# Kernel tuning notes

Hardware: AMD Instinct MI355X
Metric: run time of the kernel (lower is better)

## Reference

```python
import jax, jax.numpy as jnp
import numpy as np

IMG_H, IMG_W = 128, 128
FOCAL, NEAR, FAR = 140.0, 0.1, 10.0
RIGHT = (IMG_W - 1.0) / 2.0 * NEAR / FOCAL
TOP = RIGHT * (float(IMG_H) / IMG_W)
# row-vector GL perspective projection (v_clip = v_cam @ P), matching dirt's matrices.perspective_projection
PROJ = np.array([
    [NEAR / RIGHT, 0.0, 0.0, 0.0],
    [0.0, NEAR / TOP, 0.0, 0.0],
    [0.0, 0.0, -(FAR + NEAR) / (FAR - NEAR), -1.0],
    [0.0, 0.0, -2.0 * FAR * NEAR / (FAR - NEAR), 0.0],
], dtype=np.float32)
CHUNK = 64
EPS = 1e-9


def transform_vertices(vertices, pose):
    # vertices [N,3], pose [4,4] -> clip-space coords [N,4]
    G = jnp.array([[1.0, 0.0, 0.0], [0.0, -1.0, 0.0], [0.0, 0.0, -1.0]], jnp.float32)
    rot = G @ pose[:3, :3]
    cam_pose = pose.at[:3, :3].set(rot)
    cam_pose = cam_pose.at[1, 3].set(-pose[1, 3]).at[2, 3].set(-pose[2, 3])
    view = cam_pose.T
    vh = jnp.concatenate([vertices, jnp.ones_like(vertices[:, :1])], axis=1)
    return (vh @ view) @ jnp.asarray(PROJ)


def screen_coords(clip):
    # clip [...,4] -> pixel x (right), pixel y (down), ndc z, clip w
    w = clip[..., 3]
    x = (clip[..., 0] / w * 0.5 + 0.5) * IMG_W
    y = (0.5 - clip[..., 1] / w * 0.5) * IMG_H
    z = clip[..., 2] / w
    return x, y, z, w


def select_faces(clip, faces):
    # hard z-buffer visibility pass: per pixel, id of nearest covering face (-1 = background)
    B = clip.shape[0]
    F = faces.shape[0]
    px = jnp.arange(IMG_W, dtype=jnp.float32) + 0.5            # [W]
    py = (jnp.arange(IMG_H, dtype=jnp.float32) + 0.5)[:, None]  # [H,1]
    x, y, z, w = screen_coords(clip)                            # each [B,N]
    fchunks = faces.reshape(F // CHUNK, CHUNK, 3)
    idchunks = jnp.arange(F, dtype=jnp.int32).reshape(F // CHUNK, CHUNK)

    def body(carry, xs):
        best_z, best_f = carry
        fc, fid = xs                                  # [C,3], [C]
        xi, yi, zi, wi = x[:, fc], y[:, fc], z[:, fc], w[:, fc]   # [B,C,3]
        e4 = lambda a: a[..., None, None]             # [B,C] -> [B,C,1,1]
        x0, x1, x2 = e4(xi[..., 0]), e4(xi[..., 1]), e4(xi[..., 2])
        y0, y1, y2 = e4(yi[..., 0]), e4(yi[..., 1]), e4(yi[..., 2])
        # edge functions at pixel centers -> unnormalized barycentrics [B,C,H,W]
        e0 = (x2 - x1) * (py - y1) - (y2 - y1) * (px - x1)
        e1 = (x0 - x2) * (py - y2) - (y0 - y2) * (px - x2)
        e2 = (x1 - x0) * (py - y0) - (y1 - y0) * (px - x0)
        area = e0 + e1 + e2
        s = jnp.sign(area)
        ok = (jnp.abs(area) > EPS) & e4((wi > 1e-6).all(-1))
        inside = (e0 * s >= 0) & (e1 * s >= 0) & (e2 * s >= 0) & ok
        zpix = (e0 * e4(zi[..., 0]) + e1 * e4(zi[..., 1]) + e2 * e4(zi[..., 2])) / jnp.where(jnp.abs(area) > EPS, area, 1.0)
        inside = inside & (zpix >= -1.0) & (zpix <= 1.0)
        zc = jnp.where(inside, zpix, jnp.inf)         # [B,C,H,W]
        zmin = zc.min(axis=1)                         # [B,H,W]
        fsel = fid[zc.argmin(axis=1)]                 # [B,H,W]
        better = zmin < best_z
        return (jnp.where(better, zmin, best_z), jnp.where(better, fsel, best_f)), None

    init = (jnp.full((B, IMG_H, IMG_W), jnp.inf, jnp.float32),
            jnp.full((B, IMG_H, IMG_W), -1, jnp.int32))
    (_, best_f), _ = jax.lax.scan(body, init, (fchunks, idchunks))
    return best_f


def shade(clip, vcolors, faces, face_id):
    # differentiable perspective-correct interpolation of [mask,u,v] for the visible face
    fid = jnp.maximum(face_id, 0)                       # [B,H,W]
    vidx = faces[fid]                                   # [B,H,W,3]
    tri = jax.vmap(lambda c, vi: c[vi])(clip, vidx)     # [B,H,W,3,4]
    col = jax.vmap(lambda c, vi: c[vi])(vcolors, vidx)  # [B,H,W,3,3]
    x, y, z, w = screen_coords(tri)                     # [B,H,W,3]
    px = (jnp.arange(IMG_W, dtype=jnp.float32) + 0.5)[None, None, :]
    py = (jnp.arange(IMG_H, dtype=jnp.float32) + 0.5)[None, :, None]
    e0 = (x[..., 2] - x[..., 1]) * (py - y[..., 1]) - (y[..., 2] - y[..., 1]) * (px - x[..., 1])
    e1 = (x[..., 0] - x[..., 2]) * (py - y[..., 2]) - (y[..., 0] - y[..., 2]) * (px - x[..., 2])
    e2 = (x[..., 1] - x[..., 0]) * (py - y[..., 0]) - (y[..., 1] - y[..., 0]) * (px - x[..., 0])
    b = jnp.stack([e0, e1, e2], axis=-1)                # [B,H,W,3]
    bw = b / w                                          # perspective-correct weights
    denom = bw.sum(-1, keepdims=True)
    denom = jnp.where(jnp.abs(denom) > EPS, denom, 1.0)
    pc = bw / denom
    gbuffer = (pc[..., None] * col).sum(axis=-2)        # [B,H,W,3]
    mask = (face_id >= 0).astype(jnp.float32)[..., None]
    return gbuffer * mask


def sample_texture(texture, uv):
    # texture [TH,TW,C], uv [H,W,2]; faithful to original: clip uv, scale by full texture shape, bilinear
    th, tw = texture.shape[0], texture.shape[1]
    idx = jnp.clip(uv[..., ::-1], 0.0, 1.0) * jnp.array([th, tw], jnp.float32)
    fl = jnp.floor(idx)
    frac = idx - fl
    i = fl.astype(jnp.int32)
    iy0 = jnp.clip(i[..., 0], 0, th - 1)
    iy1 = jnp.clip(i[..., 0] + 1, 0, th - 1)
    ix0 = jnp.clip(i[..., 1], 0, tw - 1)
    ix1 = jnp.clip(i[..., 1] + 1, 0, tw - 1)
    tl = texture[iy0, ix0]; tr = texture[iy0, ix1]
    bl = texture[iy1, ix0]; br = texture[iy1, ix1]
    fy = frac[..., :1]; fx = frac[..., 1:]
    return (tl * (1.0 - fx) * (1.0 - fy) + tr * fx * (1.0 - fy)
            + bl * (1.0 - fx) * fy + br * fx * fy)


def forward(vertices, uv_map, faces, texture, poses):
    faces = faces.astype(jnp.int32)
    clip = jax.vmap(transform_vertices)(vertices, poses)         # [B,N,4]
    vcolors = jnp.concatenate([jnp.ones_like(vertices[..., :1]), uv_map], axis=-1)  # [B,N,3] = [1,u,v]
    face_id = select_faces(jax.lax.stop_gradient(clip), faces)   # [B,H,W]
    gbuffer = shade(clip, vcolors, faces, face_id)               # [B,H,W,3]
    mask_render = gbuffer[..., :1]
    uv = gbuffer[..., 1:3]
    unlit = jax.vmap(sample_texture)(texture, uv)                # [B,H,W,3]
    return unlit * mask_render


def setup_inputs():
    key = jax.random.key(0)
    k = jax.random.split(key, 5)
    B, N, F, TH, TW = 4, 4096, 8192, 2048, 2048
    vertices = jax.random.uniform(k[0], (B, N, 3), jnp.float32, -0.5, 0.5)
    uv_map = jax.random.uniform(k[1], (B, N, 2), jnp.float32)
    faces = jax.random.randint(k[2], (F, 3), 0, N, jnp.int32)
    texture = jax.random.uniform(k[3], (B, TH, TW, 3), jnp.float32)
    poses = jnp.tile(jnp.eye(4, dtype=jnp.float32)[None], (B, 1, 1))
    poses = poses.at[:, 2, 3].set(3.0)  # object ends up ~3 units in front of the GL camera
    poses = poses.at[:, 0, 3].set(jax.random.uniform(k[4], (B,), jnp.float32, -0.2, 0.2))
    return {"vertices": vertices, "uv_map": uv_map, "faces": faces, "texture": texture, "poses": poses}


def reference(vertices, uv_map, faces, texture, poses):
    return forward(vertices, uv_map, faces, texture, poses)
```

## Files before the change

### kernel.cpp

```cpp
#include <hip/hip_runtime.h>
#include <cstdint>
#include <cmath>

#define IMG_H 128
#define IMG_W 128
#define TILE 16
#define TILES_X (IMG_W / TILE)
#define TILES_Y (IMG_H / TILE)
#define NTILES (TILES_X * TILES_Y)
#define NSUB 8
#define CCH 128

constexpr double FOCAL_D = 140.0, NEAR_D = 0.1, FAR_D = 10.0;
constexpr double RIGHT_D = (IMG_W - 1.0) / 2.0 * NEAR_D / FOCAL_D;
constexpr double TOP_D   = RIGHT_D * ((double)IMG_H / (double)IMG_W);
constexpr float P00 = (float)(NEAR_D / RIGHT_D);
constexpr float P11 = (float)(NEAR_D / TOP_D);
constexpr float P22 = (float)(-(FAR_D + NEAR_D) / (FAR_D - NEAR_D));
constexpr float P32 = (float)(-2.0 * FAR_D * NEAR_D / (FAR_D - NEAR_D));

__device__ __forceinline__ unsigned long long packKey(float z, int f) {
    unsigned int zb = __float_as_uint(z);
    zb = (zb & 0x80000000u) ? ~zb : (zb | 0x80000000u);
    return ((unsigned long long)zb << 32) | (unsigned int)f;
}

__device__ __forceinline__ bool edgeAllOut(float dx, float dy, float ax, float ay,
                                           float px0, float px1, float py0, float py1,
                                           float s) {
#pragma clang fp contract(off)
    bool all = true;
    #pragma unroll
    for (int c = 0; c < 4; ++c) {
        float px = (c & 1) ? px1 : px0;
        float py = (c & 2) ? py1 : py0;
        float e = dx * (py - ay) - dy * (px - ax);
        float T = fabsf(dx) * (fabsf(py) + fabsf(ay)) + fabsf(dy) * (fabsf(px) + fabsf(ax));
        float m = 1e-5f * T + 1e-3f;
        all = all && (e * s < -m);
    }
    return all;
}

__global__ void k_vertex(const float* __restrict__ verts, const float* __restrict__ poses,
                         float4* __restrict__ vscr, int* __restrict__ cnt, int cntN,
                         int B, int N) {
#pragma clang fp contract(off)
    int id = blockIdx.x * blockDim.x + threadIdx.x;
    if (cnt && id < cntN) cnt[id] = 0;
    if (id >= B * N) return;
    int b = id / N;
    const float* v = verts + (size_t)id * 3;
    const float* P = poses + (size_t)b * 16;
    float x = v[0], y = v[1], z = v[2];
    float cp[4][4] = {
        { P[0],  P[1],  P[2],  P[3]  },
        {-P[4], -P[5], -P[6], -P[7]  },
        {-P[8], -P[9], -P[10],-P[11] },
        { P[12], P[13], P[14], P[15] }
    };
    float cam[4];
    for (int j = 0; j < 4; ++j)
        cam[j] = ((x * cp[j][0] + y * cp[j][1]) + z * cp[j][2]) + cp[j][3];
    float c0 = cam[0] * P00;
    float c1 = cam[1] * P11;
    float c2 = (cam[2] * P22) + (cam[3] * P32);
    float c3 = cam[2] * (-1.0f);
    float sx = ((c0 / c3) * 0.5f + 0.5f) * (float)IMG_W;
    float sy = (0.5f - (c1 / c3) * 0.5f) * (float)IMG_H;
    float sz = c2 / c3;
    vscr[id] = make_float4(sx, sy, sz, c3);
}

__global__ void k_bin(const int* __restrict__ faces, const float4* __restrict__ vscr,
                      float4* __restrict__ recA, float4* __restrict__ recB,
                      float4* __restrict__ recC, float4* __restrict__ recD,
                      int* __restrict__ list, int* __restrict__ cnt,
                      unsigned long long* __restrict__ keybuf,
                      int B, int N, int F) {
#pragma clang fp contract(off)
    int id = blockIdx.x * blockDim.x + threadIdx.x;
    for (int i = id; i < B * IMG_H * IMG_W; i += B * F) keybuf[i] = ~0ull;
    if (id >= B * F) return;
    int b = id / F, f = id - b * F;
    int i0 = faces[f * 3 + 0], i1 = faces[f * 3 + 1], i2 = faces[f * 3 + 2];
    float4 v0 = vscr[(size_t)b * N + i0];
    float4 v1 = vscr[(size_t)b * N + i1];
    float4 v2 = vscr[(size_t)b * N + i2];

    if (!(v0.w > 1e-6f && v1.w > 1e-6f && v2.w > 1e-6f)) return;

    float minx = fminf(v0.x, fminf(v1.x, v2.x));
    float maxx = fmaxf(v0.x, fmaxf(v1.x, v2.x));
    float miny = fminf(v0.y, fminf(v1.y, v2.y));
    float maxy = fmaxf(v0.y, fmaxf(v1.y, v2.y));
    if (!(minx <= maxx) || !(miny <= maxy)) return;
    minx = fmaxf(minx, -4.0f);  maxx = fminf(maxx, (float)IMG_W + 4.0f);
    miny = fmaxf(miny, -4.0f);  maxy = fminf(maxy, (float)IMG_H + 4.0f);
    int xlo = max(0, (int)floorf(minx) - 1);
    int xhi = min(IMG_W - 1, (int)floorf(maxx) + 1);
    int ylo = max(0, (int)floorf(miny) - 1);
    int yhi = min(IMG_H - 1, (int)floorf(maxy) + 1);
    if (xlo > xhi || ylo > yhi) return;

    float dx0 = v2.x - v1.x, dy0 = v2.y - v1.y;
    float dx1 = v0.x - v2.x, dy1 = v0.y - v2.y;
    float dx2 = v1.x - v0.x, dy2 = v1.y - v0.y;

    size_t r = (size_t)id;
    unsigned pb = (unsigned)xlo | ((unsigned)xhi << 8) | ((unsigned)ylo << 16) | ((unsigned)yhi << 24);
    recA[r] = make_float4(v1.x, v1.y, v2.x, v2.y);
    recB[r] = make_float4(v0.x, v0.y, 0.0f, 0.0f);
    recC[r] = make_float4(v0.z, v1.z, v2.z, __uint_as_float(pb));
    recD[r] = make_float4(dx0, dy0, dx1, dy1);

    int tx0 = xlo >> 4, tx1 = xhi >> 4, ty0 = ylo >> 4, ty1 = yhi >> 4;
    int sub = f & (NSUB - 1);
    int cap = (F + NSUB - 1) / NSUB;
    for (int ty = ty0; ty <= ty1; ++ty) {
        float py0 = (float)(ty << 4) + 0.5f, py1 = py0 + 15.0f;
        for (int tx = tx0; tx <= tx1; ++tx) {
            float px0 = (float)(tx << 4) + 0.5f, px1 = px0 + 15.0f;
            float ea = dx0 * (py0 - v1.y) - dy0 * (px0 - v1.x);
            float eb = dx1 * (py0 - v2.y) - dy1 * (px0 - v2.x);
            float ec = dx2 * (py0 - v0.y) - dy2 * (px0 - v0.x);
            float areaC = (ea + eb) + ec;
            float Tm = (fabsf(dx0) + fabsf(dx1) + fabsf(dx2)) * 300.0f
                     + (fabsf(dy0) + fabsf(dy1) + fabsf(dy2)) * 300.0f;
            float mA = 1e-5f * Tm + 1e-2f;
            bool cull = false;
            if (fabsf(areaC) > mA) {
                float s = (areaC > 0.0f) ? 1.0f : -1.0f;
                cull = edgeAllOut(dx0, dy0, v1.x, v1.y, px0, px1, py0, py1, s)
                    || edgeAllOut(dx1, dy1, v2.x, v2.y, px0, px1, py0, py1, s)
                    || edgeAllOut(dx2, dy2, v0.x, v0.y, px0, px1, py0, py1, s);
            }
            if (cull) continue;
            int bin = b * NTILES + ty * TILES_X + tx;
            int slot = atomicAdd(&cnt[bin * NSUB + sub], 1);
            list[((size_t)bin * NSUB + sub) * cap + slot] = f;
        }
    }
}

__global__ __launch_bounds__(256) void k_rasterChunk(const int* __restrict__ list,
        const int* __restrict__ cnt,
        const float4* __restrict__ recA, const float4* __restrict__ recB,
        const float4* __restrict__ recC, const float4* __restrict__ recD,
        unsigned long long* __restrict__ keybuf, int B, int F, int cap) {
#pragma clang fp contract(off)
    int ls = blockIdx.x;
    int n = cnt[ls];
    int base = blockIdx.y * CCH;
    if (base >= n) return;
    int m = min(CCH, n - base);
    int bin = ls >> 3;
    int b = bin / NTILES;
    int tile = bin - b * NTILES;
    const int* mylist = list + (size_t)ls * cap + base;

    int tx = tile & (TILES_X - 1), ty = tile >> 3;
    int t = threadIdx.x;
    int wv = t >> 6;
    int wx0 = (tx << 4) + ((wv & 1) << 3);
    int wy0 = (ty << 4) + ((wv >> 1) << 3);
    int x = wx0 + (t & 7);
    int y = wy0 + ((t >> 3) & 7);
    float px = (float)x + 0.5f, py = (float)y + 0.5f;
    int wx1 = wx0 + 7, wy1 = wy0 + 7;

    unsigned long long key = ~0ull;

    __shared__ float4 sA[CCH], sB[CCH], sC[CCH], sD[CCH];
    __shared__ int sfid[CCH];

    if (t < m) {
        int f = mylist[t];
        sfid[t] = f;
        size_t r = (size_t)b * F + f;
        sA[t] = recA[r]; sB[t] = recB[r]; sC[t] = recC[r]; sD[t] = recD[r];
    }
    __syncthreads();

    for (int j = 0; j < m; ++j) {
        float4 cc = sC[j];
        unsigned pb = __float_as_uint(cc.w);
        int fxlo = (int)(pb & 0xFFu), fxhi = (int)((pb >> 8) & 0xFFu);
        int fylo = (int)((pb >> 16) & 0xFFu), fyhi = (int)(pb >> 24);
        if (fxhi < wx0 || fxlo > wx1 || fyhi < wy0 || fylo > wy1) continue;
        float4 aa = sA[j], bb = sB[j], dd = sD[j];
        float e0 = dd.x * (py - aa.y) - dd.y * (px - aa.x);
        float e1 = dd.z * (py - aa.w) - dd.w * (px - aa.z);
        float dx2 = aa.x - bb.x, dy2 = aa.y - bb.y;
        float e2 = dx2 * (py - bb.y) - dy2 * (px - bb.x);
        float area = (e0 + e1) + e2;
        bool okA = fabsf(area) > 1e-9f;
        float s = (area > 0.0f) ? 1.0f : ((area < 0.0f) ? -1.0f : area);
        bool inside = (e0 * s >= 0.0f) && (e1 * s >= 0.0f) && (e2 * s >= 0.0f) && okA;
        if (__ballot(inside)) {
            float den = okA ? area : 1.0f;
            float zpix = ((e0 * cc.x + e1 * cc.y) + e2 * cc.z) / den;
            if (inside && (zpix >= -1.0f) && (zpix <= 1.0f)) {
                unsigned long long k = packKey(zpix, sfid[j]);
                key = (k < key) ? k : key;
            }
        }
    }
    if (key != ~0ull) {
        unsigned long long* ap = &keybuf[(size_t)b * (IMG_H * IMG_W) + (size_t)y * IMG_W + x];
        atomicMin(ap, key);
    }
}

__global__ __launch_bounds__(256) void k_rasterF(const int* __restrict__ faces,
                                                 const float4* __restrict__ vscr,
                                                 unsigned long long* __restrict__ keybuf,
                                                 int B, int N, int F) {
#pragma clang fp contract(off)
    int wid = __builtin_amdgcn_readfirstlane(blockIdx.x * 4 + (threadIdx.x >> 6));
    if (wid >= B * F) return;
    int b = wid / F;
    int f = wid - b * F;
    int lane = threadIdx.x & 63;

    int i0 = faces[f * 3 + 0], i1 = faces[f * 3 + 1], i2 = faces[f * 3 + 2];
    float4 v0 = vscr[(size_t)b * N + i0];
    float4 v1 = vscr[(size_t)b * N + i1];
    float4 v2 = vscr[(size_t)b * N + i2];
    if (!(v0.w > 1e-6f && v1.w > 1e-6f && v2.w > 1e-6f)) return;

    float dx0 = v2.x - v1.x, dy0 = v2.y - v1.y;
    float dx1 = v0.x - v2.x, dy1 = v0.y - v2.y;
    float dx2 = v1.x - v0.x, dy2 = v1.y - v0.y;
    float z0 = v0.z, z1 = v1.z, z2 = v2.z;

    float minx = fminf(v0.x, fminf(v1.x, v2.x));
    float maxx = fmaxf(v0.x, fmaxf(v1.x, v2.x));
    float miny = fminf(v0.y, fminf(v1.y, v2.y));
    float maxy = fmaxf(v0.y, fmaxf(v1.y, v2.y));
    if (!(minx <= maxx) || !(miny <= maxy)) return;
    minx = fmaxf(minx, -4.0f);  maxx = fminf(maxx, (float)IMG_W + 4.0f);
    miny = fmaxf(miny, -4.0f);  maxy = fminf(maxy, (float)IMG_H + 4.0f);
    int xlo = max(0, (int)floorf(minx) - 1);
    int xhi = min(IMG_W - 1, (int)floorf(maxx) + 1);
    int ylo = max(0, (int)floorf(miny) - 1);
    int yhi = min(IMG_H - 1, (int)floorf(maxy) + 1);
    if (xlo > xhi || ylo > yhi) return;

    int lx = lane & 7, lyn = lane >> 3;
    unsigned long long* kb = keybuf + (size_t)b * IMG_H * IMG_W;

    for (int y0 = ylo; y0 <= yhi; y0 += 8) {
        int y = y0 + lyn;
        bool yok = (y <= yhi);
        float py = (float)y + 0.5f;
        float pyd0 = py - v1.y, pyd1 = py - v2.y, pyd2 = py - v0.y;
        for (int x0 = xlo; x0 <= xhi; x0 += 8) {
            int x = x0 + lx;
            bool ok = yok && (x <= xhi);
            float px = (float)x + 0.5f;
            float e0 = dx0 * pyd0 - dy0 * (px - v1.x);
            float e1 = dx1 * pyd1 - dy1 * (px - v2.x);
            float e2 = dx2 * pyd2 - dy2 * (px - v0.x);
            float area = (e0 + e1) + e2;
            bool okA = fabsf(area) > 1e-9f;
            float s = (area > 0.0f) ? 1.0f : ((area < 0.0f) ? -1.0f : area);
            bool inside = (e0 * s >= 0.0f) && (e1 * s >= 0.0f) && (e2 * s >= 0.0f)
                          && okA && ok;
            if (__ballot(inside)) {
                float den = okA ? area : 1.0f;
                float zpix = ((e0 * z0 + e1 * z1) + e2 * z2) / den;
                if (inside && (zpix >= -1.0f) && (zpix <= 1.0f)) {
                    unsigned long long* ap = &kb[(size_t)y * IMG_W + x];
                    unsigned long long cur = *(const volatile unsigned long long*)ap;
                    unsigned long long k = packKey(zpix, f);
                    if (k < cur) atomicMin(ap, k);
                }
            }
        }
    }
}

__global__ void k_shade(const unsigned long long* __restrict__ keybuf,
                        const int* __restrict__ faces, const float4* __restrict__ vscr,
                        const float* __restrict__ uvmap, const float* __restrict__ tex,
                        float* __restrict__ out, int B, int N, int tside) {
#pragma clang fp contract(off)
    int id = blockIdx.x * blockDim.x + threadIdx.x;
    if (id >= B * IMG_H * IMG_W) return;
    int b = id / (IMG_H * IMG_W);
    int p = id - b * (IMG_H * IMG_W);
    int y = p / IMG_W, x = p - y * IMG_W;
    unsigned long long key = keybuf[id];
    int fid = (key == ~0ull) ? -1 : (int)(key & 0xFFFFFFFFull);
    int f = (fid < 0) ? 0 : fid;
    int i0 = faces[f * 3 + 0], i1 = faces[f * 3 + 1], i2 = faces[f * 3 + 2];
    float4 v0 = vscr[(size_t)b * N + i0];
    float4 v1 = vscr[(size_t)b * N + i1];
    float4 v2 = vscr[(size_t)b * N + i2];
    float px = (float)x + 0.5f, py = (float)y + 0.5f;
    float e0 = (v2.x - v1.x) * (py - v1.y) - (v2.y - v1.y) * (px - v1.x);
    float e1 = (v0.x - v2.x) * (py - v2.y) - (v0.y - v2.y) * (px - v2.x);
    float e2 = (v1.x - v0.x) * (py - v0.y) - (v1.y - v0.y) * (px - v0.x);
    float bw0 = e0 / v0.w, bw1 = e1 / v1.w, bw2 = e2 / v2.w;
    float den = (bw0 + bw1) + bw2;
    den = (fabsf(den) > 1e-9f) ? den : 1.0f;
    float pc0 = bw0 / den, pc1 = bw1 / den, pc2 = bw2 / den;
    float u0 = uvmap[((size_t)b * N + i0) * 2],     vv0 = uvmap[((size_t)b * N + i0) * 2 + 1];
    float u1 = uvmap[((size_t)b * N + i1) * 2],     vv1 = uvmap[((size_t)b * N + i1) * 2 + 1];
    float u2 = uvmap[((size_t)b * N + i2) * 2],     vv2 = uvmap[((size_t)b * N + i2) * 2 + 1];
    float g0 = (pc0 * 1.0f + pc1 * 1.0f) + pc2 * 1.0f;
    float g1 = (pc0 * u0 + pc1 * u1) + pc2 * u2;
    float g2 = (pc0 * vv0 + pc1 * vv1) + pc2 * vv2;
    float mask = (fid >= 0) ? 1.0f : 0.0f;
    g0 = g0 * mask; g1 = g1 * mask; g2 = g2 * mask;
    float ts = (float)tside;
    float iyf = fminf(fmaxf(g2, 0.0f), 1.0f) * ts;
    float ixf = fminf(fmaxf(g1, 0.0f), 1.0f) * ts;
    float fly = floorf(iyf), flx = floorf(ixf);
    float fy = iyf - fly, fx = ixf - flx;
    int iy = (int)fly, ix = (int)flx;
    int tmax = tside - 1;
    int iy0 = min(max(iy, 0), tmax),     iy1 = min(max(iy + 1, 0), tmax);
    int ix0 = min(max(ix, 0), tmax),     ix1 = min(max(ix + 1, 0), tmax);
    const float* tb = tex + (size_t)b * tside * tside * 3;
    const float* tl = tb + ((size_t)iy0 * tside + ix0) * 3;
    const float* tr = tb + ((size_t)iy0 * tside + ix1) * 3;
    const float* bl = tb + ((size_t)iy1 * tside + ix0) * 3;
    const float* br = tb + ((size_t)iy1 * tside + ix1) * 3;
    float omfx = 1.0f - fx, omfy = 1.0f - fy;
    float* o = out + (size_t)id * 3;
    for (int c = 0; c < 3; ++c) {
        float r = (((tl[c] * omfx) * omfy) + ((tr[c] * fx) * omfy)) + ((bl[c] * omfx) * fy);
        r = r + ((br[c] * fx) * fy);
        o[c] = r * g0;
    }
}

extern "C" void kernel_launch(void* const* d_in, const int* in_sizes, int n_in,
                              void* d_out, int out_size, void* d_ws, size_t ws_size,
                              hipStream_t stream) {
    const float* verts = (const float*)d_in[0];
    const float* uvmap = (const float*)d_in[1];
    const int*   faces = (const int*)d_in[2];
    const float* tex   = (const float*)d_in[3];
    const float* poses = (const float*)d_in[4];
    int B = in_sizes[4] / 16;
    int N = in_sizes[0] / (B * 3);
    int F = in_sizes[2] / 3;
    int texels = in_sizes[3] / (B * 3);
    int tside = (int)(sqrt((double)texels) + 0.5);

    char* ws = (char*)d_ws;
    size_t off = 0;
    float4* vscr = (float4*)(ws + off); off += (size_t)B * N * sizeof(float4);
    float4* recA = (float4*)(ws + off); off += (size_t)B * F * sizeof(float4);
    float4* recB = (float4*)(ws + off); off += (size_t)B * F * sizeof(float4);
    float4* recC = (float4*)(ws + off); off += (size_t)B * F * sizeof(float4);
    float4* recD = (float4*)(ws + off); off += (size_t)B * F * sizeof(float4);
    unsigned long long* keybuf = (unsigned long long*)(ws + off);
    size_t keybytes = (size_t)B * IMG_H * IMG_W * sizeof(unsigned long long);
    off += keybytes;
    int cap = (F + NSUB - 1) / NSUB;
    int* list = (int*)(ws + off); off += (size_t)B * NTILES * NSUB * cap * sizeof(int);
    int* cnt  = (int*)(ws + off); off += (size_t)B * NTILES * NSUB * sizeof(int);
    int cntN = B * NTILES * NSUB;

    if (ws_size >= off) {
        k_vertex<<<(B * N + 255) / 256, 256, 0, stream>>>(verts, poses, vscr, cnt, cntN, B, N);
        k_bin<<<(B * F + 255) / 256, 256, 0, stream>>>(faces, vscr, recA, recB, recC, recD,
                                                       list, cnt, keybuf, B, N, F);
        int kmax = (cap + CCH - 1) / CCH;
        dim3 rgrid(B * NTILES * NSUB, kmax);
        k_rasterChunk<<<rgrid, 256, 0, stream>>>(list, cnt, recA, recB, recC, recD,
                                                 keybuf, B, F, cap);
        k_shade<<<(B * IMG_H * IMG_W + 255) / 256, 256, 0, stream>>>(
            keybuf, faces, vscr, uvmap, tex, (float*)d_out, B, N, tside);
    } else {
        float4* vscr0 = (float4*)ws;
        unsigned long long* keybuf0 = (unsigned long long*)(ws + (size_t)B * N * sizeof(float4));
        hipMemsetAsync(keybuf0, 0xFF, keybytes, stream);
        k_vertex<<<(B * N + 255) / 256, 256, 0, stream>>>(verts, poses, vscr0, (int*)nullptr, 0, B, N);
        int nwaves = B * F;
        k_rasterF<<<(nwaves + 3) / 4, 256, 0, stream>>>(faces, vscr0, keybuf0, B, N, F);
        k_shade<<<(B * IMG_H * IMG_W + 255) / 256, 256, 0, stream>>>(
            keybuf0, faces, vscr0, uvmap, tex, (float*)d_out, B, N, tside);
    }
}
```

Measured before the change: 377.8 us.

## Merge tile sub-bins per raster block and compact face records

The raster kernel now launches one block per tile rather than per tile sub-bin. Each block concatenates the eight sub-lists and processes chunks of 256 faces instead of 128. Per-face records shrink from four float4 to two float4 plus a float2, and edge deltas are recomputed in the inner loop, which cuts global and shared memory traffic. The per-wave bounding-box overlap test is precomputed once per face as a 4-bit mask packed into the face id. This limits F to 65535 faces. The grid y dimension is now sized from F, so many blocks may launch only to exit early.

```diff
diff --git a/kernel.cpp b/kernel.cpp
--- a/kernel.cpp
+++ b/kernel.cpp
@@ -9,7 +9,7 @@
 #define TILES_Y (IMG_H / TILE)
 #define NTILES (TILES_X * TILES_Y)
 #define NSUB 8
-#define CCH 128
+#define CCH 256
 
 constexpr double FOCAL_D = 140.0, NEAR_D = 0.1, FAR_D = 10.0;
 constexpr double RIGHT_D = (IMG_W - 1.0) / 2.0 * NEAR_D / FOCAL_D;
@@ -74,7 +74,7 @@
 
 __global__ void k_bin(const int* __restrict__ faces, const float4* __restrict__ vscr,
                       float4* __restrict__ recA, float4* __restrict__ recB,
-                      float4* __restrict__ recC, float4* __restrict__ recD,
+                      float2* __restrict__ recC,
                       int* __restrict__ list, int* __restrict__ cnt,
                       unsigned long long* __restrict__ keybuf,
                       int B, int N, int F) {
@@ -110,9 +110,8 @@
     size_t r = (size_t)id;
     unsigned pb = (unsigned)xlo | ((unsigned)xhi << 8) | ((unsigned)ylo << 16) | ((unsigned)yhi << 24);
     recA[r] = make_float4(v1.x, v1.y, v2.x, v2.y);
-    recB[r] = make_float4(v0.x, v0.y, 0.0f, 0.0f);
-    recC[r] = make_float4(v0.z, v1.z, v2.z, __uint_as_float(pb));
-    recD[r] = make_float4(dx0, dy0, dx1, dy1);
+    recB[r] = make_float4(v0.x, v0.y, v0.z, v1.z);
+    recC[r] = make_float2(v2.z, __uint_as_float(pb));
 
     int tx0 = xlo >> 4, tx1 = xhi >> 4, ty0 = ylo >> 4, ty1 = yhi >> 4;
     int sub = f & (NSUB - 1);
@@ -146,18 +145,19 @@
 __global__ __launch_bounds__(256) void k_rasterChunk(const int* __restrict__ list,
         const int* __restrict__ cnt,
         const float4* __restrict__ recA, const float4* __restrict__ recB,
-        const float4* __restrict__ recC, const float4* __restrict__ recD,
+        const float2* __restrict__ recC,
         unsigned long long* __restrict__ keybuf, int B, int F, int cap) {
 #pragma clang fp contract(off)
-    int ls = blockIdx.x;
-    int n = cnt[ls];
-    int base = blockIdx.y * CCH;
-    if (base >= n) return;
-    int m = min(CCH, n - base);
-    int bin = ls >> 3;
+    int bin = blockIdx.x;
     int b = bin / NTILES;
     int tile = bin - b * NTILES;
-    const int* mylist = list + (size_t)ls * cap + base;
+    int base_ls = bin * NSUB;
+    int cnts[NSUB]; int ntot = 0;
+    #pragma unroll
+    for (int s = 0; s < NSUB; ++s) { cnts[s] = cnt[base_ls + s]; ntot += cnts[s]; }
+    int base = blockIdx.y * CCH;
+    if (base >= ntot) return;
+    int m = min(CCH, ntot - base);
 
     int tx = tile & (TILES_X - 1), ty = tile >> 3;
     int t = threadIdx.x;
@@ -167,31 +167,46 @@
     int x = wx0 + (t & 7);
     int y = wy0 + ((t >> 3) & 7);
     float px = (float)x + 0.5f, py = (float)y + 0.5f;
-    int wx1 = wx0 + 7, wy1 = wy0 + 7;
 
     unsigned long long key = ~0ull;
 
-    __shared__ float4 sA[CCH], sB[CCH], sC[CCH], sD[CCH];
-    __shared__ int sfid[CCH];
+    __shared__ float4 sA[CCH], sB[CCH];
+    __shared__ float  sC[CCH];
+    __shared__ int    sfid[CCH];
 
     if (t < m) {
-        int f = mylist[t];
-        sfid[t] = f;
+        int g = base + t;
+        int s = 0, acc = 0;
+        while (s < NSUB - 1 && g >= acc + cnts[s]) { acc += cnts[s]; ++s; }
+        int f = list[((size_t)base_ls + s) * cap + (g - acc)];
         size_t r = (size_t)b * F + f;
-        sA[t] = recA[r]; sB[t] = recB[r]; sC[t] = recC[r]; sD[t] = recD[r];
-    }
-    __syncthreads();
-
-    for (int j = 0; j < m; ++j) {
-        float4 cc = sC[j];
-        unsigned pb = __float_as_uint(cc.w);
+        float4 A = recA[r]; float4 Bv = recB[r]; float2 C = recC[r];
+        unsigned pb = __float_as_uint(C.y);
         int fxlo = (int)(pb & 0xFFu), fxhi = (int)((pb >> 8) & 0xFFu);
         int fylo = (int)((pb >> 16) & 0xFFu), fyhi = (int)(pb >> 24);
-        if (fxhi < wx0 || fxlo > wx1 || fyhi < wy0 || fylo > wy1) continue;
-        float4 aa = sA[j], bb = sB[j], dd = sD[j];
-        float e0 = dd.x * (py - aa.y) - dd.y * (px - aa.x);
-        float e1 = dd.z * (py - aa.w) - dd.w * (px - aa.z);
+        int msk = 0;
+        #pragma unroll
+        for (int q = 0; q < 4; ++q) {
+            int qx0 = (tx << 4) + ((q & 1) << 3);
+            int qy0 = (ty << 4) + ((q >> 1) << 3);
+            bool ov = !(fxhi < qx0 || fxlo > qx0 + 7 || fyhi < qy0 || fylo > qy0 + 7);
+            msk |= (int)ov << q;
+        }
+        sA[t] = A; sB[t] = Bv; sC[t] = C.x;
+        sfid[t] = (msk << 16) | f;
+    }
+    __syncthreads();
+
+    for (int j = 0; j < m; ++j) {
+        int sf = sfid[j];
+        if (!((sf >> (16 + wv)) & 1)) continue;
+        float4 aa = sA[j], bb = sB[j];
+        float z2 = sC[j];
+        float dx0 = aa.z - aa.x, dy0 = aa.w - aa.y;
+        float dx1 = bb.x - aa.z, dy1 = bb.y - aa.w;
         float dx2 = aa.x - bb.x, dy2 = aa.y - bb.y;
+        float e0 = dx0 * (py - aa.y) - dy0 * (px - aa.x);
+        float e1 = dx1 * (py - aa.w) - dy1 * (px - aa.z);
         float e2 = dx2 * (py - bb.y) - dy2 * (px - bb.x);
         float area = (e0 + e1) + e2;
         bool okA = fabsf(area) > 1e-9f;
@@ -199,9 +214,9 @@
         bool inside = (e0 * s >= 0.0f) && (e1 * s >= 0.0f) && (e2 * s >= 0.0f) && okA;
         if (__ballot(inside)) {
             float den = okA ? area : 1.0f;
-            float zpix = ((e0 * cc.x + e1 * cc.y) + e2 * cc.z) / den;
+            float zpix = ((e0 * bb.z + e1 * bb.w) + e2 * z2) / den;
             if (inside && (zpix >= -1.0f) && (zpix <= 1.0f)) {
-                unsigned long long k = packKey(zpix, sfid[j]);
+                unsigned long long k = packKey(zpix, sf & 0xFFFF);
                 key = (k < key) ? k : key;
             }
         }
@@ -356,8 +371,7 @@
     float4* vscr = (float4*)(ws + off); off += (size_t)B * N * sizeof(float4);
     float4* recA = (float4*)(ws + off); off += (size_t)B * F * sizeof(float4);
     float4* recB = (float4*)(ws + off); off += (size_t)B * F * sizeof(float4);
-    float4* recC = (float4*)(ws + off); off += (size_t)B * F * sizeof(float4);
-    float4* recD = (float4*)(ws + off); off += (size_t)B * F * sizeof(float4);
+    float2* recC = (float2*)(ws + off); off += (size_t)B * F * sizeof(float2);
     unsigned long long* keybuf = (unsigned long long*)(ws + off);
     size_t keybytes = (size_t)B * IMG_H * IMG_W * sizeof(unsigned long long);
     off += keybytes;
@@ -366,13 +380,13 @@
     int* cnt  = (int*)(ws + off); off += (size_t)B * NTILES * NSUB * sizeof(int);
     int cntN = B * NTILES * NSUB;
 
-    if (ws_size >= off) {
+    if (ws_size >= off && F <= 0xFFFF) {
         k_vertex<<<(B * N + 255) / 256, 256, 0, stream>>>(verts, poses, vscr, cnt, cntN, B, N);
-        k_bin<<<(B * F + 255) / 256, 256, 0, stream>>>(faces, vscr, recA, recB, recC, recD,
+        k_bin<<<(B * F + 255) / 256, 256, 0, stream>>>(faces, vscr, recA, recB, recC,
                                                        list, cnt, keybuf, B, N, F);
-        int kmax = (cap + CCH - 1) / CCH;
-        dim3 rgrid(B * NTILES * NSUB, kmax);
-        k_rasterChunk<<<rgrid, 256, 0, stream>>>(list, cnt, recA, recB, recC, recD,
+        int kmax = (F + CCH - 1) / CCH;
+        dim3 rgrid(B * NTILES, kmax);
+        k_rasterChunk<<<rgrid, 256, 0, stream>>>(list, cnt, recA, recB, recC,
                                                  keybuf, B, F, cap);
         k_shade<<<(B * IMG_H * IMG_W + 255) / 256, 256, 0, stream>>>(
             keybuf, faces, vscr, uvmap, tex, (float*)d_out, B, N, tside);
```

After: 498.8 us. +32.0%, slower.
